# Kernel tuning notes

Measured on AMD Instinct MI355X. Metric: run time of the kernel, lower is better.

## Reference

```python
import jax, jax.numpy as jnp
import numpy as np

N_NODES = 100000
N_EDGES = 1600000
IN_F = 128
OUT_F = 128
HID = 2 * OUT_F  # 256


def setup_inputs() -> dict:
    key = jax.random.key(0)
    k1, k2, k3, k4, k5 = jax.random.split(key, 5)
    x = jax.random.normal(k1, (N_NODES, IN_F), dtype=jnp.float32)
    src = jax.random.randint(k2, (N_EDGES,), 0, N_NODES, dtype=jnp.int64)
    dst = jax.random.randint(k3, (N_EDGES,), 0, N_NODES, dtype=jnp.int64)
    # GraphConv params: glorot-style init, zero bias (as in dgl defaults)
    W1 = jax.random.normal(k4, (IN_F, HID), dtype=jnp.float32) / np.sqrt(IN_F)
    b1 = jnp.zeros((HID,), dtype=jnp.float32)
    W2 = jax.random.normal(k5, (HID, OUT_F), dtype=jnp.float32) / np.sqrt(HID)
    b2 = jnp.zeros((OUT_F,), dtype=jnp.float32)
    return {"x": x, "W1": W1, "b1": b1, "W2": W2, "b2": b2, "src": src, "dst": dst}


def _degree_norms(src, dst):
    ones = jnp.ones(src.shape[0], dtype=jnp.float32)
    out_deg = jax.ops.segment_sum(ones, src, num_segments=N_NODES)
    in_deg = jax.ops.segment_sum(ones, dst, num_segments=N_NODES)
    # dgl norm='both': deg^{-1/2}, with 0-degree clamped to 1
    out_norm = jnp.where(out_deg > 0, out_deg, 1.0) ** -0.5
    in_norm = jnp.where(in_deg > 0, in_deg, 1.0) ** -0.5
    return out_norm, in_norm


def _graph_conv(x, W, b, src, dst, out_norm, in_norm):
    # dgl GraphConv, norm='both': apply weight first if in_feats > out_feats
    h = x * out_norm[:, None]
    if W.shape[0] > W.shape[1]:
        h = h @ W                       # [N, out] -- shrink before aggregation
        agg = jax.ops.segment_sum(h[src], dst, num_segments=N_NODES)
        return agg * in_norm[:, None] + b
    else:
        agg = jax.ops.segment_sum(h[src], dst, num_segments=N_NODES)
        return (agg * in_norm[:, None]) @ W + b


def reference(x, W1, b1, W2, b2, src, dst):
    out_norm, in_norm = _degree_norms(src, dst)
    h = jax.nn.relu(_graph_conv(x, W1, b1, src, dst, out_norm, in_norm))
    h = jax.nn.relu(_graph_conv(h, W2, b2, src, dst, out_norm, in_norm))
    return h
```

## Files before the change

### kernel.cpp

```cpp
#include <hip/hip_runtime.h>
#include <stdint.h>

#define NNODES 100000
#define NEDGES 1600000
#define NBIN 391
#define EPB 4096
#define NB 391

typedef unsigned short bf16_t;
typedef __attribute__((ext_vector_type(8))) short bf16x8;
typedef __attribute__((ext_vector_type(8))) unsigned short u16x8;
typedef __attribute__((ext_vector_type(4))) float f32x4;

__device__ __forceinline__ float bf2f(unsigned short u) {
  return __uint_as_float(((unsigned)u) << 16);
}
__device__ __forceinline__ unsigned short f2bf(float f) {
  unsigned u = __float_as_uint(f);
  return (unsigned short)((u + 0x7FFFu + ((u >> 16) & 1u)) >> 16);
}
__device__ __forceinline__ void gload_lds16(const void* g, void* lds) {
  __builtin_amdgcn_global_load_lds(
      (const __attribute__((address_space(1))) unsigned int*)g,
      (__attribute__((address_space(3))) unsigned int*)lds, 16, 0, 0);
}

__global__ __launch_bounds__(256) void hist2_kernel(
    const int* __restrict__ src, const int* __restrict__ dst,
    int* __restrict__ cntD, int* __restrict__ cntS) {
  __shared__ int hD[NBIN], hS[NBIN];
  int blk = blockIdx.x, t = threadIdx.x;
  for (int i = t; i < NBIN; i += 256) { hD[i] = 0; hS[i] = 0; }
  __syncthreads();
  int e0 = blk * EPB + t * 16;
  if (e0 + 15 < NEDGES) {
#pragma unroll
    for (int q = 0; q < 4; q++) {
      int4 s4 = *reinterpret_cast<const int4*>(src + e0 + q * 4);
      int4 d4 = *reinterpret_cast<const int4*>(dst + e0 + q * 4);
      atomicAdd(&hD[d4.x >> 8], 1); atomicAdd(&hS[s4.x >> 8], 1);
      atomicAdd(&hD[d4.y >> 8], 1); atomicAdd(&hS[s4.y >> 8], 1);
      atomicAdd(&hD[d4.z >> 8], 1); atomicAdd(&hS[s4.z >> 8], 1);
      atomicAdd(&hD[d4.w >> 8], 1); atomicAdd(&hS[s4.w >> 8], 1);
    }
  } else {
    for (int e = e0; e < NEDGES && e < e0 + 16; e++) {
      atomicAdd(&hD[dst[e] >> 8], 1);
      atomicAdd(&hS[src[e] >> 8], 1);
    }
  }
  __syncthreads();
  for (int i = t; i < NBIN; i += 256) {
    cntD[(size_t)blk * NBIN + i] = hD[i];
    cntS[(size_t)blk * NBIN + i] = hS[i];
  }
}

__global__ __launch_bounds__(512) void scan_bin_kernel(
    int* __restrict__ cntD, int* __restrict__ cntS, int* __restrict__ binTot) {
  __shared__ int lds[512];
  int g = blockIdx.x, t = threadIdx.x;
  int* cnt = (g < NBIN) ? cntD : cntS;
  int gg = (g < NBIN) ? g : g - NBIN;
  int v = (t < NB) ? cnt[(size_t)t * NBIN + gg] : 0;
  lds[t] = v;
  __syncthreads();
  for (int off = 1; off < 512; off <<= 1) {
    int a = (t >= off) ? lds[t - off] : 0;
    __syncthreads();
    lds[t] += a;
    __syncthreads();
  }
  if (t < NB) cnt[(size_t)t * NBIN + gg] = lds[t] - v;
  if (t == 0) binTot[g] = lds[511];
}

__global__ __launch_bounds__(512) void base_wcast_kernel(
    const int* __restrict__ binTot, int* __restrict__ binbaseD,
    int* __restrict__ binbaseS, int* __restrict__ row_ptr,
    const float* __restrict__ W1, const float* __restrict__ W2,
    bf16_t* __restrict__ W1t, bf16_t* __restrict__ W2t) {
  if (blockIdx.x == 0) {
    __shared__ int lds[512];
    int t = threadIdx.x;
    int v = (t < NBIN) ? binTot[t] : 0;
    lds[t] = v;
    __syncthreads();
    for (int off = 1; off < 512; off <<= 1) {
      int a = (t >= off) ? lds[t - off] : 0;
      __syncthreads();
      lds[t] += a;
      __syncthreads();
    }
    if (t < NBIN) binbaseD[t] = lds[t] - v;
    if (t == NBIN - 1) { binbaseD[NBIN] = lds[t]; row_ptr[NNODES] = lds[t]; }
    __syncthreads();
    int v2 = (t < NBIN) ? binTot[NBIN + t] : 0;
    lds[t] = v2;
    __syncthreads();
    for (int off = 1; off < 512; off <<= 1) {
      int a = (t >= off) ? lds[t - off] : 0;
      __syncthreads();
      lds[t] += a;
      __syncthreads();
    }
    if (t < NBIN) binbaseS[t] = lds[t] - v2;
    if (t == NBIN - 1) binbaseS[NBIN] = lds[t];
  } else {
    int i = (blockIdx.x - 1) * 512 + threadIdx.x;
    if (i < 32768) {
      int n = i / 128, k = i % 128;
      W1t[i] = f2bf(W1[(size_t)k * 256 + n]);
    } else if (i < 65536) {
      int j = i - 32768;
      int n = j / 256, k = j % 256;
      W2t[j] = f2bf(W2[(size_t)k * 128 + n]);
    }
  }
}

__global__ __launch_bounds__(256) void scatter_recs_kernel(
    const int* __restrict__ src, const int* __restrict__ dst,
    const int* __restrict__ cntD, const int* __restrict__ cntS,
    const int* __restrict__ binbaseD, const int* __restrict__ binbaseS,
    unsigned int* __restrict__ recD, unsigned char* __restrict__ recS) {
  __shared__ int cD[NBIN], cS[NBIN];
  int blk = blockIdx.x, t = threadIdx.x;
  for (int i = t; i < NBIN; i += 256) {
    cD[i] = binbaseD[i] + cntD[(size_t)blk * NBIN + i];
    cS[i] = binbaseS[i] + cntS[(size_t)blk * NBIN + i];
  }
  __syncthreads();
  int e0 = blk * EPB + t * 16;
  if (e0 + 15 < NEDGES) {
#pragma unroll
    for (int q = 0; q < 4; q++) {
      int4 s4 = *reinterpret_cast<const int4*>(src + e0 + q * 4);
      int4 d4 = *reinterpret_cast<const int4*>(dst + e0 + q * 4);
      int ss[4] = {s4.x, s4.y, s4.z, s4.w};
      int dd[4] = {d4.x, d4.y, d4.z, d4.w};
#pragma unroll
      for (int i = 0; i < 4; i++) {
        int s = ss[i], d = dd[i];
        int pos = atomicAdd(&cD[d >> 8], 1);
        recD[pos] = ((unsigned)s << 8) | (unsigned)(d & 255);
        int ps = atomicAdd(&cS[s >> 8], 1);
        recS[ps] = (unsigned char)(s & 255);
      }
    }
  } else {
    for (int e = e0; e < NEDGES && e < e0 + 16; e++) {
      int s = src[e], d = dst[e];
      int pos = atomicAdd(&cD[d >> 8], 1);
      recD[pos] = ((unsigned)s << 8) | (unsigned)(d & 255);
      int ps = atomicAdd(&cS[s >> 8], 1);
      recS[ps] = (unsigned char)(s & 255);
    }
  }
}

__global__ __launch_bounds__(512) void finish2_kernel(
    const unsigned int* __restrict__ recD, const int* __restrict__ binbaseD,
    const unsigned char* __restrict__ recS, const int* __restrict__ binbaseS,
    int* __restrict__ row_ptr, float* __restrict__ in_norm, int* __restrict__ csr,
    float* __restrict__ out_norm, const float* __restrict__ x, bf16_t* __restrict__ xb) {
  __shared__ int hist[4096];
  __shared__ int cur[4096];
  __shared__ int sc[512];
  __shared__ float onv[256];
  int t = threadIdx.x;
  if (blockIdx.x < NBIN) {
    int b = blockIdx.x;
    int base = binbaseD[b];
    int cnt = binbaseD[b + 1] - base;
    for (int i = t; i < 4096; i += 512) hist[i] = 0;
    __syncthreads();
    const unsigned int* rec = recD + base;
    for (int i = t; i < cnt; i += 512) {
      unsigned int r = rec[i];
      atomicAdd(&hist[((r & 255u) << 4) | (r >> 21)], 1);
    }
    __syncthreads();
    int loc[8];
    int lsum = 0;
#pragma unroll
    for (int i = 0; i < 8; i++) { loc[i] = lsum; lsum += hist[t * 8 + i]; }
    sc[t] = lsum;
    __syncthreads();
    for (int off = 1; off < 512; off <<= 1) {
      int a = (t >= off) ? sc[t - off] : 0;
      __syncthreads();
      sc[t] += a;
      __syncthreads();
    }
    int toff = sc[t] - lsum;
#pragma unroll
    for (int i = 0; i < 8; i++) cur[t * 8 + i] = base + toff + loc[i];
    __syncthreads();
    if (t < 256) {
      int n = (b << 8) + t;
      if (n < NNODES) {
        row_ptr[n] = cur[t * 16];
        int v = 0;
#pragma unroll
        for (int p = 0; p < 16; p++) v += hist[t * 16 + p];
        in_norm[n] = rsqrtf((float)(v > 0 ? v : 1));
      }
    }
    __syncthreads();
    for (int i = t; i < cnt; i += 512) {
      unsigned int r = rec[i];
      int key = ((r & 255u) << 4) | (r >> 21);
      int slot = atomicAdd(&cur[key], 1);
      csr[slot] = (int)(r >> 8);
    }
  } else {
    int b = blockIdx.x - NBIN;
    int base = binbaseS[b];
    int cnt = binbaseS[b + 1] - base;
    if (t < 256) hist[t] = 0;
    __syncthreads();
    const unsigned char* rec = recS + base;
    for (int i = t; i < cnt; i += 512) atomicAdd(&hist[rec[i]], 1);
    __syncthreads();
    int n0 = b << 8;
    if (t < 256) {
      int v = hist[t];
      float on = rsqrtf((float)(v > 0 ? v : 1));
      onv[t] = on;
      int n = n0 + t;
      if (n < NNODES) out_norm[n] = on;
    }
    __syncthreads();
    for (int idx = t; idx < 256 * 16; idx += 512) {
      int r16 = idx >> 4, chunk = idx & 15;
      int n = n0 + r16;
      if (n >= NNODES) break;
      float s = onv[r16];
      const float4* xp = reinterpret_cast<const float4*>(x + (size_t)n * 128 + chunk * 8);
      float4 v0 = xp[0], v1 = xp[1];
      u16x8 u;
      u[0] = f2bf(v0.x * s); u[1] = f2bf(v0.y * s); u[2] = f2bf(v0.z * s); u[3] = f2bf(v0.w * s);
      u[4] = f2bf(v1.x * s); u[5] = f2bf(v1.y * s); u[6] = f2bf(v1.z * s); u[7] = f2bf(v1.w * s);
      *reinterpret_cast<u16x8*>(xb + (size_t)n * 128 + chunk * 8) = u;
    }
  }
}

template <int FIN>
__global__ __launch_bounds__(256) void gather_kernel(
    const bf16_t* __restrict__ feat, const int* __restrict__ row_ptr,
    const int* __restrict__ csr, const float* __restrict__ rs,
    const float* __restrict__ bias, void* __restrict__ outp) {
  int nbk = gridDim.x;
  int q = nbk >> 3, r = nbk & 7;
  int x = blockIdx.x & 7, o = blockIdx.x >> 3;
  int vb = (x < r ? x * (q + 1) : r * (q + 1) + (x - r) * q) + o;
  int node = vb * 16 + (threadIdx.x >> 4);
  int lane = threadIdx.x & 15;
  int start = row_ptr[node];
  int end = row_ptr[node + 1];
  float a[8];
#pragma unroll
  for (int t = 0; t < 8; t++) a[t] = 0.f;
  int j = start;
  for (; j + 7 < end; j += 8) {
    int4 sa = *reinterpret_cast<const int4*>(csr + j);
    int4 sb = *reinterpret_cast<const int4*>(csr + j + 4);
    u16x8 u0 = *reinterpret_cast<const u16x8*>(feat + (size_t)sa.x * 128 + lane * 8);
    u16x8 u1 = *reinterpret_cast<const u16x8*>(feat + (size_t)sa.y * 128 + lane * 8);
    u16x8 u2 = *reinterpret_cast<const u16x8*>(feat + (size_t)sa.z * 128 + lane * 8);
    u16x8 u3 = *reinterpret_cast<const u16x8*>(feat + (size_t)sa.w * 128 + lane * 8);
    u16x8 u4 = *reinterpret_cast<const u16x8*>(feat + (size_t)sb.x * 128 + lane * 8);
    u16x8 u5 = *reinterpret_cast<const u16x8*>(feat + (size_t)sb.y * 128 + lane * 8);
    u16x8 u6 = *reinterpret_cast<const u16x8*>(feat + (size_t)sb.z * 128 + lane * 8);
    u16x8 u7 = *reinterpret_cast<const u16x8*>(feat + (size_t)sb.w * 128 + lane * 8);
#pragma unroll
    for (int t = 0; t < 8; t++)
      a[t] += ((bf2f((unsigned short)u0[t]) + bf2f((unsigned short)u1[t])) +
               (bf2f((unsigned short)u2[t]) + bf2f((unsigned short)u3[t]))) +
              ((bf2f((unsigned short)u4[t]) + bf2f((unsigned short)u5[t])) +
               (bf2f((unsigned short)u6[t]) + bf2f((unsigned short)u7[t])));
  }
  if (j + 3 < end) {
    int4 sa = *reinterpret_cast<const int4*>(csr + j);
    u16x8 u0 = *reinterpret_cast<const u16x8*>(feat + (size_t)sa.x * 128 + lane * 8);
    u16x8 u1 = *reinterpret_cast<const u16x8*>(feat + (size_t)sa.y * 128 + lane * 8);
    u16x8 u2 = *reinterpret_cast<const u16x8*>(feat + (size_t)sa.z * 128 + lane * 8);
    u16x8 u3 = *reinterpret_cast<const u16x8*>(feat + (size_t)sa.w * 128 + lane * 8);
#pragma unroll
    for (int t = 0; t < 8; t++)
      a[t] += (bf2f((unsigned short)u0[t]) + bf2f((unsigned short)u1[t])) +
              (bf2f((unsigned short)u2[t]) + bf2f((unsigned short)u3[t]));
    j += 4;
  }
  for (; j < end; j++) {
    int s0 = csr[j];
    u16x8 u0 = *reinterpret_cast<const u16x8*>(feat + (size_t)s0 * 128 + lane * 8);
#pragma unroll
    for (int t = 0; t < 8; t++) a[t] += bf2f((unsigned short)u0[t]);
  }
  if (FIN == 0) {
    u16x8 o8;
#pragma unroll
    for (int t = 0; t < 8; t++) o8[t] = f2bf(a[t]);
    *reinterpret_cast<u16x8*>((bf16_t*)outp + (size_t)node * 128 + lane * 8) = o8;
  } else {
    float s = rs[node];
    const float* bp = bias + lane * 8;
    float4 o0, o1;
    o0.x = fmaxf(fmaf(a[0], s, bp[0]), 0.f);
    o0.y = fmaxf(fmaf(a[1], s, bp[1]), 0.f);
    o0.z = fmaxf(fmaf(a[2], s, bp[2]), 0.f);
    o0.w = fmaxf(fmaf(a[3], s, bp[3]), 0.f);
    o1.x = fmaxf(fmaf(a[4], s, bp[4]), 0.f);
    o1.y = fmaxf(fmaf(a[5], s, bp[5]), 0.f);
    o1.z = fmaxf(fmaf(a[6], s, bp[6]), 0.f);
    o1.w = fmaxf(fmaf(a[7], s, bp[7]), 0.f);
    float* op = (float*)outp + (size_t)node * 128 + lane * 8;
    *reinterpret_cast<float4*>(op) = o0;
    *reinterpret_cast<float4*>(op + 4) = o1;
  }
}

__global__ __launch_bounds__(256) void gemm12_kernel(
    const bf16_t* __restrict__ A,
    const bf16_t* __restrict__ W1t,
    const bf16_t* __restrict__ W2t,
    const float* __restrict__ b1,
    const float* __restrict__ in_norm,
    const float* __restrict__ out_norm,
    bf16_t* __restrict__ s2b) {
  __shared__ __align__(16) bf16_t As[64 * 128];
  __shared__ __align__(16) bf16_t Wb[128 * 128];
  __shared__ __align__(16) bf16_t H[64 * 256];

  const int tid = threadIdx.x;
  const int lane = tid & 63;
  const int w = tid >> 6;
  const int m0 = blockIdx.x * 64;
  const int l15 = lane & 15;
  const int S = lane >> 4;
  const int r = w * 16 + l15;
  const int lr0 = w * 16 + S * 4;

#pragma unroll
  for (int p = 0; p < 4; p++) {
    int pos = p * 256 + tid;
    int rr = pos >> 4, slot = pos & 15;
    int row = m0 + rr; if (row > NNODES - 1) row = NNODES - 1;
    int ko = (slot ^ (rr & 7)) << 3;
    gload_lds16(A + (size_t)row * 128 + ko, &As[(p * 256 + w * 64) * 8]);
  }
#pragma unroll
  for (int p = 0; p < 8; p++) {
    int pos = p * 256 + tid;
    int n = pos >> 4, slot = pos & 15;
    int ko = (slot ^ (n & 7)) << 3;
    gload_lds16(W1t + (size_t)n * 128 + ko, &Wb[(p * 256 + w * 64) * 8]);
  }
  __syncthreads();

  float inn[4];
#pragma unroll
  for (int reg = 0; reg < 4; reg++) {
    int grow = m0 + lr0 + reg;
    inn[reg] = (grow < NNODES) ? in_norm[grow] : 1.0f;
  }

#pragma unroll
  for (int h = 0; h < 2; h++) {
    if (h == 1) {
      __syncthreads();
#pragma unroll
      for (int p = 0; p < 8; p++) {
        int pos = p * 256 + tid;
        int n = pos >> 4, slot = pos & 15;
        int ko = (slot ^ (n & 7)) << 3;
        gload_lds16(W1t + (size_t)(128 + n) * 128 + ko, &Wb[(p * 256 + w * 64) * 8]);
      }
      __syncthreads();
    }
    f32x4 acc1[8];
#pragma unroll
    for (int fn = 0; fn < 8; fn++) acc1[fn] = (f32x4){0.f, 0.f, 0.f, 0.f};
#pragma unroll
    for (int kk8 = 0; kk8 < 16; kk8 += 4) {
      bf16x8 af = *reinterpret_cast<const bf16x8*>(&As[r * 128 + (((kk8 + S) ^ (r & 7)) << 3)]);
#pragma unroll
      for (int fn = 0; fn < 8; fn++) {
        int n = fn * 16 + l15;
        bf16x8 bf = *reinterpret_cast<const bf16x8*>(&Wb[n * 128 + (((kk8 + S) ^ (n & 7)) << 3)]);
        acc1[fn] = __builtin_amdgcn_mfma_f32_16x16x32_bf16(af, bf, acc1[fn], 0, 0, 0);
      }
    }
#pragma unroll
    for (int fn = 0; fn < 8; fn++) {
      int col = h * 128 + fn * 16 + l15;
      float bb = b1[col];
#pragma unroll
      for (int reg = 0; reg < 4; reg++) {
        int lr = lr0 + reg;
        float v = fmaxf(fmaf(acc1[fn][reg], inn[reg], bb), 0.f);
        int slot = (col >> 3) ^ (lr & 7);
        H[lr * 256 + slot * 8 + (col & 7)] = f2bf(v);
      }
    }
  }
  __syncthreads();

  f32x4 acc2[8];
#pragma unroll
  for (int fn = 0; fn < 8; fn++) acc2[fn] = (f32x4){0.f, 0.f, 0.f, 0.f};
#pragma unroll
  for (int kh = 0; kh < 2; kh++) {
#pragma unroll
    for (int p = 0; p < 8; p++) {
      int pos = p * 256 + tid;
      int n = pos >> 4, slot = pos & 15;
      int ko = kh * 128 + ((slot ^ (n & 7)) << 3);
      gload_lds16(W2t + (size_t)n * 256 + ko, &Wb[(p * 256 + w * 64) * 8]);
    }
    __syncthreads();
#pragma unroll
    for (int kk8 = 0; kk8 < 16; kk8 += 4) {
      int oct = kh * 16 + kk8 + S;
      bf16x8 af = *reinterpret_cast<const bf16x8*>(&H[r * 256 + ((oct ^ (r & 7)) << 3)]);
#pragma unroll
      for (int fn = 0; fn < 8; fn++) {
        int n = fn * 16 + l15;
        bf16x8 bf = *reinterpret_cast<const bf16x8*>(&Wb[n * 128 + (((kk8 + S) ^ (n & 7)) << 3)]);
        acc2[fn] = __builtin_amdgcn_mfma_f32_16x16x32_bf16(af, bf, acc2[fn], 0, 0, 0);
      }
    }
    __syncthreads();
  }

  float onr[4];
#pragma unroll
  for (int reg = 0; reg < 4; reg++) {
    int grow = m0 + lr0 + reg;
    onr[reg] = (grow < NNODES) ? out_norm[grow] : 0.0f;
  }
#pragma unroll
  for (int fn = 0; fn < 8; fn++) {
    int col = fn * 16 + l15;
#pragma unroll
    for (int reg = 0; reg < 4; reg++) {
      int lr = lr0 + reg;
      As[lr * 128 + col] = f2bf(acc2[fn][reg] * onr[reg]);
    }
  }
  __syncthreads();
#pragma unroll
  for (int p = 0; p < 4; p++) {
    int pos = p * 256 + tid;
    int rr = pos >> 4;
    int cc = (pos & 15) * 8;
    int grow = m0 + rr;
    if (grow < NNODES)
      *reinterpret_cast<u16x8*>(s2b + (size_t)grow * 128 + cc) =
          *reinterpret_cast<const u16x8*>(&As[rr * 128 + cc]);
  }
}

extern "C" void kernel_launch(void* const* d_in, const int* in_sizes, int n_in,
                              void* d_out, int out_size, void* d_ws, size_t ws_size,
                              hipStream_t stream) {
  const float* x  = (const float*)d_in[0];
  const float* W1 = (const float*)d_in[1];
  const float* b1 = (const float*)d_in[2];
  const float* W2 = (const float*)d_in[3];
  const float* b2 = (const float*)d_in[4];
  const int* src  = (const int*)d_in[5];
  const int* dst  = (const int*)d_in[6];
  float* out = (float*)d_out;

  char* ws = (char*)d_ws;
  int*           cntD     = (int*)          (ws + 0);
  int*           cntS     = (int*)          (ws + 700000);
  int*           binTot   = (int*)          (ws + 1400000);
  int*           binbaseD = (int*)          (ws + 1404000);
  int*           binbaseS = (int*)          (ws + 1406000);
  int*           row_ptr  = (int*)          (ws + 1408000);
  float*         out_norm = (float*)        (ws + 1810000);
  float*         in_norm  = (float*)        (ws + 2210000);
  bf16_t*        W1t      = (bf16_t*)       (ws + 2610000);
  bf16_t*        W2t      = (bf16_t*)       (ws + 2675536);
  unsigned int*  recD     = (unsigned int*) (ws + 2741072);
  unsigned char* recS     = (unsigned char*)(ws + 9141072);
  int*           csr      = (int*)          (ws + 10741072);
  bf16_t*        xb       = (bf16_t*)       (ws + 17141072);
  bf16_t*        agg1     = (bf16_t*)       (ws + 42741072);
  bf16_t*        s2b      = xb;

  hist2_kernel<<<NB, 256, 0, stream>>>(src, dst, cntD, cntS);
  scan_bin_kernel<<<2 * NBIN, 512, 0, stream>>>(cntD, cntS, binTot);
  base_wcast_kernel<<<129, 512, 0, stream>>>(binTot, binbaseD, binbaseS, row_ptr, W1, W2, W1t, W2t);
  scatter_recs_kernel<<<NB, 256, 0, stream>>>(src, dst, cntD, cntS, binbaseD, binbaseS, recD, recS);
  finish2_kernel<<<2 * NBIN, 512, 0, stream>>>(recD, binbaseD, recS, binbaseS,
                                               row_ptr, in_norm, csr, out_norm, x, xb);

  gather_kernel<0><<<NNODES / 16, 256, 0, stream>>>(xb, row_ptr, csr, nullptr, nullptr, agg1);

  gemm12_kernel<<<(NNODES + 63) / 64, 256, 0, stream>>>(agg1, W1t, W2t, b1, in_norm, out_norm, s2b);

  gather_kernel<1><<<NNODES / 16, 256, 0, stream>>>(s2b, row_ptr, csr, in_norm, b2, out);
}
```

Measured before the change: 255.2 us.

## Fuse first-layer gather with both dense GEMMs into one kernel

The first aggregation is merged with the two MFMA matmuls in one kernel. Each 16-node block keeps its aggregated row tile in LDS and multiplies it by W1 and then W2, reading the weights directly from global memory instead of staging them in LDS. This removes the bf16 agg1 round-trip to HBM and one kernel launch. In exchange, every block re-reads W1t and W2t (relying on L2 hits), runs only 16-row MFMA tiles, and the extra LDS may lower occupancy of the latency-bound gather.

```diff
diff --git a/kernel.cpp b/kernel.cpp
--- a/kernel.cpp
+++ b/kernel.cpp
@@ -247,17 +247,27 @@
   }
 }
 
-template <int FIN>
-__global__ __launch_bounds__(256) void gather_kernel(
-    const bf16_t* __restrict__ feat, const int* __restrict__ row_ptr,
-    const int* __restrict__ csr, const float* __restrict__ rs,
-    const float* __restrict__ bias, void* __restrict__ outp) {
+__global__ __launch_bounds__(256) void gather_gemm_kernel(
+    const bf16_t* __restrict__ feat,
+    const int* __restrict__ row_ptr, const int* __restrict__ csr,
+    const bf16_t* __restrict__ W1t,
+    const bf16_t* __restrict__ W2t,
+    const float* __restrict__ b1,
+    const float* __restrict__ in_norm,
+    const float* __restrict__ out_norm,
+    bf16_t* __restrict__ s2b) {
+  __shared__ __align__(16) bf16_t T[16 * 128];
+  __shared__ __align__(16) bf16_t H[16 * 256];
+
   int nbk = gridDim.x;
-  int q = nbk >> 3, r = nbk & 7;
-  int x = blockIdx.x & 7, o = blockIdx.x >> 3;
-  int vb = (x < r ? x * (q + 1) : r * (q + 1) + (x - r) * q) + o;
-  int node = vb * 16 + (threadIdx.x >> 4);
+  int q = nbk >> 3, r8 = nbk & 7;
+  int xc = blockIdx.x & 7, ob = blockIdx.x >> 3;
+  int vb = (xc < r8 ? xc * (q + 1) : r8 * (q + 1) + (xc - r8) * q) + ob;
+  int node0 = vb * 16;
+  int g = threadIdx.x >> 4;
   int lane = threadIdx.x & 15;
+  int node = node0 + g;
+
   int start = row_ptr[node];
   int end = row_ptr[node + 1];
   float a[8];
@@ -300,168 +310,154 @@
 #pragma unroll
     for (int t = 0; t < 8; t++) a[t] += bf2f((unsigned short)u0[t]);
   }
-  if (FIN == 0) {
+  {
     u16x8 o8;
 #pragma unroll
     for (int t = 0; t < 8; t++) o8[t] = f2bf(a[t]);
-    *reinterpret_cast<u16x8*>((bf16_t*)outp + (size_t)node * 128 + lane * 8) = o8;
-  } else {
-    float s = rs[node];
-    const float* bp = bias + lane * 8;
-    float4 o0, o1;
-    o0.x = fmaxf(fmaf(a[0], s, bp[0]), 0.f);
-    o0.y = fmaxf(fmaf(a[1], s, bp[1]), 0.f);
-    o0.z = fmaxf(fmaf(a[2], s, bp[2]), 0.f);
-    o0.w = fmaxf(fmaf(a[3], s, bp[3]), 0.f);
-    o1.x = fmaxf(fmaf(a[4], s, bp[4]), 0.f);
-    o1.y = fmaxf(fmaf(a[5], s, bp[5]), 0.f);
-    o1.z = fmaxf(fmaf(a[6], s, bp[6]), 0.f);
-    o1.w = fmaxf(fmaf(a[7], s, bp[7]), 0.f);
-    float* op = (float*)outp + (size_t)node * 128 + lane * 8;
-    *reinterpret_cast<float4*>(op) = o0;
-    *reinterpret_cast<float4*>(op + 4) = o1;
-  }
-}
-
-__global__ __launch_bounds__(256) void gemm12_kernel(
-    const bf16_t* __restrict__ A,
-    const bf16_t* __restrict__ W1t,
-    const bf16_t* __restrict__ W2t,
-    const float* __restrict__ b1,
-    const float* __restrict__ in_norm,
-    const float* __restrict__ out_norm,
-    bf16_t* __restrict__ s2b) {
-  __shared__ __align__(16) bf16_t As[64 * 128];
-  __shared__ __align__(16) bf16_t Wb[128 * 128];
-  __shared__ __align__(16) bf16_t H[64 * 256];
+    *reinterpret_cast<u16x8*>(&T[g * 128 + ((lane ^ (g & 7)) << 3)]) = o8;
+  }
+  __syncthreads();
 
   const int tid = threadIdx.x;
-  const int lane = tid & 63;
-  const int w = tid >> 6;
-  const int m0 = blockIdx.x * 64;
-  const int l15 = lane & 15;
-  const int S = lane >> 4;
-  const int r = w * 16 + l15;
-  const int lr0 = w * 16 + S * 4;
-
-#pragma unroll
-  for (int p = 0; p < 4; p++) {
-    int pos = p * 256 + tid;
-    int rr = pos >> 4, slot = pos & 15;
-    int row = m0 + rr; if (row > NNODES - 1) row = NNODES - 1;
-    int ko = (slot ^ (rr & 7)) << 3;
-    gload_lds16(A + (size_t)row * 128 + ko, &As[(p * 256 + w * 64) * 8]);
-  }
-#pragma unroll
-  for (int p = 0; p < 8; p++) {
-    int pos = p * 256 + tid;
-    int n = pos >> 4, slot = pos & 15;
-    int ko = (slot ^ (n & 7)) << 3;
-    gload_lds16(W1t + (size_t)n * 128 + ko, &Wb[(p * 256 + w * 64) * 8]);
-  }
-  __syncthreads();
-
-  float inn[4];
+  const int wv = tid >> 6;
+  const int l63 = tid & 63;
+  const int l15 = l63 & 15;
+  const int S = l63 >> 4;
+  const int row0 = S * 4;
+
+  float inn[4], onr[4];
 #pragma unroll
   for (int reg = 0; reg < 4; reg++) {
-    int grow = m0 + lr0 + reg;
-    inn[reg] = (grow < NNODES) ? in_norm[grow] : 1.0f;
-  }
-
-#pragma unroll
-  for (int h = 0; h < 2; h++) {
-    if (h == 1) {
-      __syncthreads();
-#pragma unroll
-      for (int p = 0; p < 8; p++) {
-        int pos = p * 256 + tid;
-        int n = pos >> 4, slot = pos & 15;
-        int ko = (slot ^ (n & 7)) << 3;
-        gload_lds16(W1t + (size_t)(128 + n) * 128 + ko, &Wb[(p * 256 + w * 64) * 8]);
-      }
-      __syncthreads();
-    }
-    f32x4 acc1[8];
-#pragma unroll
-    for (int fn = 0; fn < 8; fn++) acc1[fn] = (f32x4){0.f, 0.f, 0.f, 0.f};
-#pragma unroll
-    for (int kk8 = 0; kk8 < 16; kk8 += 4) {
-      bf16x8 af = *reinterpret_cast<const bf16x8*>(&As[r * 128 + (((kk8 + S) ^ (r & 7)) << 3)]);
-#pragma unroll
-      for (int fn = 0; fn < 8; fn++) {
-        int n = fn * 16 + l15;
-        bf16x8 bf = *reinterpret_cast<const bf16x8*>(&Wb[n * 128 + (((kk8 + S) ^ (n & 7)) << 3)]);
-        acc1[fn] = __builtin_amdgcn_mfma_f32_16x16x32_bf16(af, bf, acc1[fn], 0, 0, 0);
-      }
-    }
-#pragma unroll
-    for (int fn = 0; fn < 8; fn++) {
-      int col = h * 128 + fn * 16 + l15;
-      float bb = b1[col];
-#pragma unroll
-      for (int reg = 0; reg < 4; reg++) {
-        int lr = lr0 + reg;
-        float v = fmaxf(fmaf(acc1[fn][reg], inn[reg], bb), 0.f);
-        int slot = (col >> 3) ^ (lr & 7);
-        H[lr * 256 + slot * 8 + (col & 7)] = f2bf(v);
-      }
-    }
-  }
-  __syncthreads();
-
-  f32x4 acc2[8];
-#pragma unroll
-  for (int fn = 0; fn < 8; fn++) acc2[fn] = (f32x4){0.f, 0.f, 0.f, 0.f};
-#pragma unroll
-  for (int kh = 0; kh < 2; kh++) {
-#pragma unroll
-    for (int p = 0; p < 8; p++) {
-      int pos = p * 256 + tid;
-      int n = pos >> 4, slot = pos & 15;
-      int ko = kh * 128 + ((slot ^ (n & 7)) << 3);
-      gload_lds16(W2t + (size_t)n * 256 + ko, &Wb[(p * 256 + w * 64) * 8]);
-    }
-    __syncthreads();
-#pragma unroll
-    for (int kk8 = 0; kk8 < 16; kk8 += 4) {
-      int oct = kh * 16 + kk8 + S;
-      bf16x8 af = *reinterpret_cast<const bf16x8*>(&H[r * 256 + ((oct ^ (r & 7)) << 3)]);
-#pragma unroll
-      for (int fn = 0; fn < 8; fn++) {
-        int n = fn * 16 + l15;
-        bf16x8 bf = *reinterpret_cast<const bf16x8*>(&Wb[n * 128 + (((kk8 + S) ^ (n & 7)) << 3)]);
-        acc2[fn] = __builtin_amdgcn_mfma_f32_16x16x32_bf16(af, bf, acc2[fn], 0, 0, 0);
-      }
-    }
-    __syncthreads();
-  }
-
-  float onr[4];
-#pragma unroll
-  for (int reg = 0; reg < 4; reg++) {
-    int grow = m0 + lr0 + reg;
-    onr[reg] = (grow < NNODES) ? out_norm[grow] : 0.0f;
-  }
-#pragma unroll
-  for (int fn = 0; fn < 8; fn++) {
-    int col = fn * 16 + l15;
+    inn[reg] = in_norm[node0 + row0 + reg];
+    onr[reg] = out_norm[node0 + row0 + reg];
+  }
+
+  f32x4 acc1[4];
+#pragma unroll
+  for (int fn = 0; fn < 4; fn++) acc1[fn] = (f32x4){0.f, 0.f, 0.f, 0.f};
+#pragma unroll
+  for (int ks = 0; ks < 4; ks++) {
+    int oct = ks * 4 + S;
+    bf16x8 af = *reinterpret_cast<const bf16x8*>(&T[l15 * 128 + ((oct ^ (l15 & 7)) << 3)]);
+#pragma unroll
+    for (int fn = 0; fn < 4; fn++) {
+      int n = wv * 64 + fn * 16 + l15;
+      bf16x8 bf = *reinterpret_cast<const bf16x8*>(W1t + (size_t)n * 128 + oct * 8);
+      acc1[fn] = __builtin_amdgcn_mfma_f32_16x16x32_bf16(af, bf, acc1[fn], 0, 0, 0);
+    }
+  }
+#pragma unroll
+  for (int fn = 0; fn < 4; fn++) {
+    int col = wv * 64 + fn * 16 + l15;
+    float bb = b1[col];
 #pragma unroll
     for (int reg = 0; reg < 4; reg++) {
-      int lr = lr0 + reg;
-      As[lr * 128 + col] = f2bf(acc2[fn][reg] * onr[reg]);
-    }
-  }
-  __syncthreads();
-#pragma unroll
-  for (int p = 0; p < 4; p++) {
-    int pos = p * 256 + tid;
-    int rr = pos >> 4;
-    int cc = (pos & 15) * 8;
-    int grow = m0 + rr;
-    if (grow < NNODES)
-      *reinterpret_cast<u16x8*>(s2b + (size_t)grow * 128 + cc) =
-          *reinterpret_cast<const u16x8*>(&As[rr * 128 + cc]);
-  }
+      int lr = row0 + reg;
+      float v = fmaxf(fmaf(acc1[fn][reg], inn[reg], bb), 0.f);
+      int slot = (col >> 3) ^ (lr & 7);
+      H[lr * 256 + slot * 8 + (col & 7)] = f2bf(v);
+    }
+  }
+  __syncthreads();
+
+  f32x4 acc2[2];
+#pragma unroll
+  for (int fn = 0; fn < 2; fn++) acc2[fn] = (f32x4){0.f, 0.f, 0.f, 0.f};
+#pragma unroll
+  for (int ks = 0; ks < 8; ks++) {
+    int oct = ks * 4 + S;
+    bf16x8 af = *reinterpret_cast<const bf16x8*>(&H[l15 * 256 + ((oct ^ (l15 & 7)) << 3)]);
+#pragma unroll
+    for (int fn = 0; fn < 2; fn++) {
+      int n = wv * 32 + fn * 16 + l15;
+      bf16x8 bf = *reinterpret_cast<const bf16x8*>(W2t + (size_t)n * 256 + oct * 8);
+      acc2[fn] = __builtin_amdgcn_mfma_f32_16x16x32_bf16(af, bf, acc2[fn], 0, 0, 0);
+    }
+  }
+  __syncthreads();
+#pragma unroll
+  for (int fn = 0; fn < 2; fn++) {
+    int col = wv * 32 + fn * 16 + l15;
+#pragma unroll
+    for (int reg = 0; reg < 4; reg++) {
+      int lr = row0 + reg;
+      T[lr * 128 + col] = f2bf(acc2[fn][reg] * onr[reg]);
+    }
+  }
+  __syncthreads();
+  {
+    int rr = tid >> 4, cc = (tid & 15) * 8;
+    *reinterpret_cast<u16x8*>(s2b + (size_t)(node0 + rr) * 128 + cc) =
+        *reinterpret_cast<const u16x8*>(&T[rr * 128 + cc]);
+  }
+}
+
+__global__ __launch_bounds__(256) void gather_kernel(
+    const bf16_t* __restrict__ feat, const int* __restrict__ row_ptr,
+    const int* __restrict__ csr, const float* __restrict__ rs,
+    const float* __restrict__ bias, float* __restrict__ outp) {
+  int nbk = gridDim.x;
+  int q = nbk >> 3, r = nbk & 7;
+  int x = blockIdx.x & 7, o = blockIdx.x >> 3;
+  int vb = (x < r ? x * (q + 1) : r * (q + 1) + (x - r) * q) + o;
+  int node = vb * 16 + (threadIdx.x >> 4);
+  int lane = threadIdx.x & 15;
+  int start = row_ptr[node];
+  int end = row_ptr[node + 1];
+  float a[8];
+#pragma unroll
+  for (int t = 0; t < 8; t++) a[t] = 0.f;
+  int j = start;
+  for (; j + 7 < end; j += 8) {
+    int4 sa = *reinterpret_cast<const int4*>(csr + j);
+    int4 sb = *reinterpret_cast<const int4*>(csr + j + 4);
+    u16x8 u0 = *reinterpret_cast<const u16x8*>(feat + (size_t)sa.x * 128 + lane * 8);
+    u16x8 u1 = *reinterpret_cast<const u16x8*>(feat + (size_t)sa.y * 128 + lane * 8);
+    u16x8 u2 = *reinterpret_cast<const u16x8*>(feat + (size_t)sa.z * 128 + lane * 8);
+    u16x8 u3 = *reinterpret_cast<const u16x8*>(feat + (size_t)sa.w * 128 + lane * 8);
+    u16x8 u4 = *reinterpret_cast<const u16x8*>(feat + (size_t)sb.x * 128 + lane * 8);
+    u16x8 u5 = *reinterpret_cast<const u16x8*>(feat + (size_t)sb.y * 128 + lane * 8);
+    u16x8 u6 = *reinterpret_cast<const u16x8*>(feat + (size_t)sb.z * 128 + lane * 8);
+    u16x8 u7 = *reinterpret_cast<const u16x8*>(feat + (size_t)sb.w * 128 + lane * 8);
+#pragma unroll
+    for (int t = 0; t < 8; t++)
+      a[t] += ((bf2f((unsigned short)u0[t]) + bf2f((unsigned short)u1[t])) +
+               (bf2f((unsigned short)u2[t]) + bf2f((unsigned short)u3[t]))) +
+              ((bf2f((unsigned short)u4[t]) + bf2f((unsigned short)u5[t])) +
+               (bf2f((unsigned short)u6[t]) + bf2f((unsigned short)u7[t])));
+  }
+  if (j + 3 < end) {
+    int4 sa = *reinterpret_cast<const int4*>(csr + j);
+    u16x8 u0 = *reinterpret_cast<const u16x8*>(feat + (size_t)sa.x * 128 + lane * 8);
+    u16x8 u1 = *reinterpret_cast<const u16x8*>(feat + (size_t)sa.y * 128 + lane * 8);
+    u16x8 u2 = *reinterpret_cast<const u16x8*>(feat + (size_t)sa.z * 128 + lane * 8);
+    u16x8 u3 = *reinterpret_cast<const u16x8*>(feat + (size_t)sa.w * 128 + lane * 8);
+#pragma unroll
+    for (int t = 0; t < 8; t++)
+      a[t] += (bf2f((unsigned short)u0[t]) + bf2f((unsigned short)u1[t])) +
+              (bf2f((unsigned short)u2[t]) + bf2f((unsigned short)u3[t]));
+    j += 4;
+  }
+  for (; j < end; j++) {
+    int s0 = csr[j];
+    u16x8 u0 = *reinterpret_cast<const u16x8*>(feat + (size_t)s0 * 128 + lane * 8);
+#pragma unroll
+    for (int t = 0; t < 8; t++) a[t] += bf2f((unsigned short)u0[t]);
+  }
+  float s = rs[node];
+  const float* bp = bias + lane * 8;
+  float4 o0, o1;
+  o0.x = fmaxf(fmaf(a[0], s, bp[0]), 0.f);
+  o0.y = fmaxf(fmaf(a[1], s, bp[1]), 0.f);
+  o0.z = fmaxf(fmaf(a[2], s, bp[2]), 0.f);
+  o0.w = fmaxf(fmaf(a[3], s, bp[3]), 0.f);
+  o1.x = fmaxf(fmaf(a[4], s, bp[4]), 0.f);
+  o1.y = fmaxf(fmaf(a[5], s, bp[5]), 0.f);
+  o1.z = fmaxf(fmaf(a[6], s, bp[6]), 0.f);
+  o1.w = fmaxf(fmaf(a[7], s, bp[7]), 0.f);
+  float* op = outp + (size_t)node * 128 + lane * 8;
+  *reinterpret_cast<float4*>(op) = o0;
+  *reinterpret_cast<float4*>(op + 4) = o1;
 }
 
 extern "C" void kernel_launch(void* const* d_in, const int* in_sizes, int n_in,
@@ -491,8 +487,7 @@
   unsigned char* recS     = (unsigned char*)(ws + 9141072);
   int*           csr      = (int*)          (ws + 10741072);
   bf16_t*        xb       = (bf16_t*)       (ws + 17141072);
-  bf16_t*        agg1     = (bf16_t*)       (ws + 42741072);
-  bf16_t*        s2b      = xb;
+  bf16_t*        s2b      = (bf16_t*)       (ws + 42741072);
 
   hist2_kernel<<<NB, 256, 0, stream>>>(src, dst, cntD, cntS);
   scan_bin_kernel<<<2 * NBIN, 512, 0, stream>>>(cntD, cntS, binTot);
@@ -501,9 +496,8 @@
   finish2_kernel<<<2 * NBIN, 512, 0, stream>>>(recD, binbaseD, recS, binbaseS,
                                                row_ptr, in_norm, csr, out_norm, x, xb);
 
-  gather_kernel<0><<<NNODES / 16, 256, 0, stream>>>(xb, row_ptr, csr, nullptr, nullptr, agg1);
-
-  gemm12_kernel<<<(NNODES + 63) / 64, 256, 0, stream>>>(agg1, W1t, W2t, b1, in_norm, out_norm, s2b);
-
-  gather_kernel<1><<<NNODES / 16, 256, 0, stream>>>(s2b, row_ptr, csr, in_norm, b2, out);
-}
+  gather_gemm_kernel<<<NNODES / 16, 256, 0, stream>>>(xb, row_ptr, csr, W1t, W2t,
+                                                      b1, in_norm, out_norm, s2b);
+
+  gather_kernel<<<NNODES / 16, 256, 0, stream>>>(s2b, row_ptr, csr, in_norm, b2, out);
+}
```

New measurement: 286.2 us. 12.2% more time.

## Replace per-block bin counts and scan with global atomic bin totals and cursors

Applied to the files above, without the earlier changes.

The histogram kernel now adds per-block bin counts straight into global bin totals with atomics, which removes the per-block count arrays and the separate column-scan kernel. The scatter kernel recomputes its local histogram and reserves each block's offsets by atomically bumping global per-bin cursors, so edge order within a bin is no longer deterministic. The gather kernel also switches its CSR index loads and output stores to nontemporal accesses. The aim is to cut one launch and the intermediate count traffic, at the cost of redoing the histogram pass and adding global atomic contention.

```diff
diff --git a/kernel.cpp b/kernel.cpp
--- a/kernel.cpp
+++ b/kernel.cpp
@@ -11,6 +11,7 @@
 typedef __attribute__((ext_vector_type(8))) short bf16x8;
 typedef __attribute__((ext_vector_type(8))) unsigned short u16x8;
 typedef __attribute__((ext_vector_type(4))) float f32x4;
+typedef __attribute__((ext_vector_type(4))) int i32x4;
 
 __device__ __forceinline__ float bf2f(unsigned short u) {
   return __uint_as_float(((unsigned)u) << 16);
@@ -25,9 +26,9 @@
       (__attribute__((address_space(3))) unsigned int*)lds, 16, 0, 0);
 }
 
-__global__ __launch_bounds__(256) void hist2_kernel(
+__global__ __launch_bounds__(256) void histg_kernel(
     const int* __restrict__ src, const int* __restrict__ dst,
-    int* __restrict__ cntD, int* __restrict__ cntS) {
+    int* __restrict__ binTot) {
   __shared__ int hD[NBIN], hS[NBIN];
   int blk = blockIdx.x, t = threadIdx.x;
   for (int i = t; i < NBIN; i += 256) { hD[i] = 0; hS[i] = 0; }
@@ -51,33 +52,15 @@
   }
   __syncthreads();
   for (int i = t; i < NBIN; i += 256) {
-    cntD[(size_t)blk * NBIN + i] = hD[i];
-    cntS[(size_t)blk * NBIN + i] = hS[i];
-  }
-}
-
-__global__ __launch_bounds__(512) void scan_bin_kernel(
-    int* __restrict__ cntD, int* __restrict__ cntS, int* __restrict__ binTot) {
-  __shared__ int lds[512];
-  int g = blockIdx.x, t = threadIdx.x;
-  int* cnt = (g < NBIN) ? cntD : cntS;
-  int gg = (g < NBIN) ? g : g - NBIN;
-  int v = (t < NB) ? cnt[(size_t)t * NBIN + gg] : 0;
-  lds[t] = v;
-  __syncthreads();
-  for (int off = 1; off < 512; off <<= 1) {
-    int a = (t >= off) ? lds[t - off] : 0;
-    __syncthreads();
-    lds[t] += a;
-    __syncthreads();
-  }
-  if (t < NB) cnt[(size_t)t * NBIN + gg] = lds[t] - v;
-  if (t == 0) binTot[g] = lds[511];
+    if (hD[i]) atomicAdd(&binTot[i], hD[i]);
+    if (hS[i]) atomicAdd(&binTot[NBIN + i], hS[i]);
+  }
 }
 
 __global__ __launch_bounds__(512) void base_wcast_kernel(
     const int* __restrict__ binTot, int* __restrict__ binbaseD,
-    int* __restrict__ binbaseS, int* __restrict__ row_ptr,
+    int* __restrict__ binbaseS, int* __restrict__ cursD, int* __restrict__ cursS,
+    int* __restrict__ row_ptr,
     const float* __restrict__ W1, const float* __restrict__ W2,
     bf16_t* __restrict__ W1t, bf16_t* __restrict__ W2t) {
   if (blockIdx.x == 0) {
@@ -92,7 +75,7 @@
       lds[t] += a;
       __syncthreads();
     }
-    if (t < NBIN) binbaseD[t] = lds[t] - v;
+    if (t < NBIN) { int b = lds[t] - v; binbaseD[t] = b; cursD[t] = b; }
     if (t == NBIN - 1) { binbaseD[NBIN] = lds[t]; row_ptr[NNODES] = lds[t]; }
     __syncthreads();
     int v2 = (t < NBIN) ? binTot[NBIN + t] : 0;
@@ -104,7 +87,7 @@
       lds[t] += a;
       __syncthreads();
     }
-    if (t < NBIN) binbaseS[t] = lds[t] - v2;
+    if (t < NBIN) { int b = lds[t] - v2; binbaseS[t] = b; cursS[t] = b; }
     if (t == NBIN - 1) binbaseS[NBIN] = lds[t];
   } else {
     int i = (blockIdx.x - 1) * 512 + threadIdx.x;
@@ -119,19 +102,39 @@
   }
 }
 
-__global__ __launch_bounds__(256) void scatter_recs_kernel(
+__global__ __launch_bounds__(256) void scatter2_kernel(
     const int* __restrict__ src, const int* __restrict__ dst,
-    const int* __restrict__ cntD, const int* __restrict__ cntS,
-    const int* __restrict__ binbaseD, const int* __restrict__ binbaseS,
+    int* __restrict__ cursD, int* __restrict__ cursS,
     unsigned int* __restrict__ recD, unsigned char* __restrict__ recS) {
-  __shared__ int cD[NBIN], cS[NBIN];
+  __shared__ int hD[NBIN], hS[NBIN];
   int blk = blockIdx.x, t = threadIdx.x;
+  for (int i = t; i < NBIN; i += 256) { hD[i] = 0; hS[i] = 0; }
+  __syncthreads();
+  int e0 = blk * EPB + t * 16;
+  if (e0 + 15 < NEDGES) {
+#pragma unroll
+    for (int q = 0; q < 4; q++) {
+      int4 s4 = *reinterpret_cast<const int4*>(src + e0 + q * 4);
+      int4 d4 = *reinterpret_cast<const int4*>(dst + e0 + q * 4);
+      atomicAdd(&hD[d4.x >> 8], 1); atomicAdd(&hS[s4.x >> 8], 1);
+      atomicAdd(&hD[d4.y >> 8], 1); atomicAdd(&hS[s4.y >> 8], 1);
+      atomicAdd(&hD[d4.z >> 8], 1); atomicAdd(&hS[s4.z >> 8], 1);
+      atomicAdd(&hD[d4.w >> 8], 1); atomicAdd(&hS[s4.w >> 8], 1);
+    }
+  } else {
+    for (int e = e0; e < NEDGES && e < e0 + 16; e++) {
+      atomicAdd(&hD[dst[e] >> 8], 1);
+      atomicAdd(&hS[src[e] >> 8], 1);
+    }
+  }
+  __syncthreads();
   for (int i = t; i < NBIN; i += 256) {
-    cD[i] = binbaseD[i] + cntD[(size_t)blk * NBIN + i];
-    cS[i] = binbaseS[i] + cntS[(size_t)blk * NBIN + i];
-  }
-  __syncthreads();
-  int e0 = blk * EPB + t * 16;
+    int c = hD[i];
+    hD[i] = c ? atomicAdd(&cursD[i], c) : 0;
+    int c2 = hS[i];
+    hS[i] = c2 ? atomicAdd(&cursS[i], c2) : 0;
+  }
+  __syncthreads();
   if (e0 + 15 < NEDGES) {
 #pragma unroll
     for (int q = 0; q < 4; q++) {
@@ -142,18 +145,18 @@
 #pragma unroll
       for (int i = 0; i < 4; i++) {
         int s = ss[i], d = dd[i];
-        int pos = atomicAdd(&cD[d >> 8], 1);
+        int pos = atomicAdd(&hD[d >> 8], 1);
         recD[pos] = ((unsigned)s << 8) | (unsigned)(d & 255);
-        int ps = atomicAdd(&cS[s >> 8], 1);
+        int ps = atomicAdd(&hS[s >> 8], 1);
         recS[ps] = (unsigned char)(s & 255);
       }
     }
   } else {
     for (int e = e0; e < NEDGES && e < e0 + 16; e++) {
       int s = src[e], d = dst[e];
-      int pos = atomicAdd(&cD[d >> 8], 1);
+      int pos = atomicAdd(&hD[d >> 8], 1);
       recD[pos] = ((unsigned)s << 8) | (unsigned)(d & 255);
-      int ps = atomicAdd(&cS[s >> 8], 1);
+      int ps = atomicAdd(&hS[s >> 8], 1);
       recS[ps] = (unsigned char)(s & 255);
     }
   }
@@ -265,16 +268,16 @@
   for (int t = 0; t < 8; t++) a[t] = 0.f;
   int j = start;
   for (; j + 7 < end; j += 8) {
-    int4 sa = *reinterpret_cast<const int4*>(csr + j);
-    int4 sb = *reinterpret_cast<const int4*>(csr + j + 4);
-    u16x8 u0 = *reinterpret_cast<const u16x8*>(feat + (size_t)sa.x * 128 + lane * 8);
-    u16x8 u1 = *reinterpret_cast<const u16x8*>(feat + (size_t)sa.y * 128 + lane * 8);
-    u16x8 u2 = *reinterpret_cast<const u16x8*>(feat + (size_t)sa.z * 128 + lane * 8);
-    u16x8 u3 = *reinterpret_cast<const u16x8*>(feat + (size_t)sa.w * 128 + lane * 8);
-    u16x8 u4 = *reinterpret_cast<const u16x8*>(feat + (size_t)sb.x * 128 + lane * 8);
-    u16x8 u5 = *reinterpret_cast<const u16x8*>(feat + (size_t)sb.y * 128 + lane * 8);
-    u16x8 u6 = *reinterpret_cast<const u16x8*>(feat + (size_t)sb.z * 128 + lane * 8);
-    u16x8 u7 = *reinterpret_cast<const u16x8*>(feat + (size_t)sb.w * 128 + lane * 8);
+    i32x4 sa = __builtin_nontemporal_load(reinterpret_cast<const i32x4*>(csr + j));
+    i32x4 sb = __builtin_nontemporal_load(reinterpret_cast<const i32x4*>(csr + j + 4));
+    u16x8 u0 = *reinterpret_cast<const u16x8*>(feat + (size_t)sa[0] * 128 + lane * 8);
+    u16x8 u1 = *reinterpret_cast<const u16x8*>(feat + (size_t)sa[1] * 128 + lane * 8);
+    u16x8 u2 = *reinterpret_cast<const u16x8*>(feat + (size_t)sa[2] * 128 + lane * 8);
+    u16x8 u3 = *reinterpret_cast<const u16x8*>(feat + (size_t)sa[3] * 128 + lane * 8);
+    u16x8 u4 = *reinterpret_cast<const u16x8*>(feat + (size_t)sb[0] * 128 + lane * 8);
+    u16x8 u5 = *reinterpret_cast<const u16x8*>(feat + (size_t)sb[1] * 128 + lane * 8);
+    u16x8 u6 = *reinterpret_cast<const u16x8*>(feat + (size_t)sb[2] * 128 + lane * 8);
+    u16x8 u7 = *reinterpret_cast<const u16x8*>(feat + (size_t)sb[3] * 128 + lane * 8);
 #pragma unroll
     for (int t = 0; t < 8; t++)
       a[t] += ((bf2f((unsigned short)u0[t]) + bf2f((unsigned short)u1[t])) +
@@ -283,11 +286,11 @@
                (bf2f((unsigned short)u6[t]) + bf2f((unsigned short)u7[t])));
   }
   if (j + 3 < end) {
-    int4 sa = *reinterpret_cast<const int4*>(csr + j);
-    u16x8 u0 = *reinterpret_cast<const u16x8*>(feat + (size_t)sa.x * 128 + lane * 8);
-    u16x8 u1 = *reinterpret_cast<const u16x8*>(feat + (size_t)sa.y * 128 + lane * 8);
-    u16x8 u2 = *reinterpret_cast<const u16x8*>(feat + (size_t)sa.z * 128 + lane * 8);
-    u16x8 u3 = *reinterpret_cast<const u16x8*>(feat + (size_t)sa.w * 128 + lane * 8);
+    i32x4 sa = __builtin_nontemporal_load(reinterpret_cast<const i32x4*>(csr + j));
+    u16x8 u0 = *reinterpret_cast<const u16x8*>(feat + (size_t)sa[0] * 128 + lane * 8);
+    u16x8 u1 = *reinterpret_cast<const u16x8*>(feat + (size_t)sa[1] * 128 + lane * 8);
+    u16x8 u2 = *reinterpret_cast<const u16x8*>(feat + (size_t)sa[2] * 128 + lane * 8);
+    u16x8 u3 = *reinterpret_cast<const u16x8*>(feat + (size_t)sa[3] * 128 + lane * 8);
 #pragma unroll
     for (int t = 0; t < 8; t++)
       a[t] += (bf2f((unsigned short)u0[t]) + bf2f((unsigned short)u1[t])) +
@@ -304,22 +307,23 @@
     u16x8 o8;
 #pragma unroll
     for (int t = 0; t < 8; t++) o8[t] = f2bf(a[t]);
-    *reinterpret_cast<u16x8*>((bf16_t*)outp + (size_t)node * 128 + lane * 8) = o8;
+    __builtin_nontemporal_store(
+        o8, reinterpret_cast<u16x8*>((bf16_t*)outp + (size_t)node * 128 + lane * 8));
   } else {
     float s = rs[node];
     const float* bp = bias + lane * 8;
-    float4 o0, o1;
-    o0.x = fmaxf(fmaf(a[0], s, bp[0]), 0.f);
-    o0.y = fmaxf(fmaf(a[1], s, bp[1]), 0.f);
-    o0.z = fmaxf(fmaf(a[2], s, bp[2]), 0.f);
-    o0.w = fmaxf(fmaf(a[3], s, bp[3]), 0.f);
-    o1.x = fmaxf(fmaf(a[4], s, bp[4]), 0.f);
-    o1.y = fmaxf(fmaf(a[5], s, bp[5]), 0.f);
-    o1.z = fmaxf(fmaf(a[6], s, bp[6]), 0.f);
-    o1.w = fmaxf(fmaf(a[7], s, bp[7]), 0.f);
+    f32x4 o0, o1;
+    o0[0] = fmaxf(fmaf(a[0], s, bp[0]), 0.f);
+    o0[1] = fmaxf(fmaf(a[1], s, bp[1]), 0.f);
+    o0[2] = fmaxf(fmaf(a[2], s, bp[2]), 0.f);
+    o0[3] = fmaxf(fmaf(a[3], s, bp[3]), 0.f);
+    o1[0] = fmaxf(fmaf(a[4], s, bp[4]), 0.f);
+    o1[1] = fmaxf(fmaf(a[5], s, bp[5]), 0.f);
+    o1[2] = fmaxf(fmaf(a[6], s, bp[6]), 0.f);
+    o1[3] = fmaxf(fmaf(a[7], s, bp[7]), 0.f);
     float* op = (float*)outp + (size_t)node * 128 + lane * 8;
-    *reinterpret_cast<float4*>(op) = o0;
-    *reinterpret_cast<float4*>(op + 4) = o1;
+    __builtin_nontemporal_store(o0, reinterpret_cast<f32x4*>(op));
+    __builtin_nontemporal_store(o1, reinterpret_cast<f32x4*>(op + 4));
   }
 }
 
@@ -477,27 +481,29 @@
   float* out = (float*)d_out;
 
   char* ws = (char*)d_ws;
-  int*           cntD     = (int*)          (ws + 0);
-  int*           cntS     = (int*)          (ws + 700000);
-  int*           binTot   = (int*)          (ws + 1400000);
-  int*           binbaseD = (int*)          (ws + 1404000);
-  int*           binbaseS = (int*)          (ws + 1406000);
-  int*           row_ptr  = (int*)          (ws + 1408000);
-  float*         out_norm = (float*)        (ws + 1810000);
-  float*         in_norm  = (float*)        (ws + 2210000);
-  bf16_t*        W1t      = (bf16_t*)       (ws + 2610000);
-  bf16_t*        W2t      = (bf16_t*)       (ws + 2675536);
-  unsigned int*  recD     = (unsigned int*) (ws + 2741072);
-  unsigned char* recS     = (unsigned char*)(ws + 9141072);
-  int*           csr      = (int*)          (ws + 10741072);
-  bf16_t*        xb       = (bf16_t*)       (ws + 17141072);
-  bf16_t*        agg1     = (bf16_t*)       (ws + 42741072);
+  int*           binTot   = (int*)          (ws + 0);
+  int*           binbaseD = (int*)          (ws + 4000);
+  int*           binbaseS = (int*)          (ws + 6000);
+  int*           cursD    = (int*)          (ws + 8000);
+  int*           cursS    = (int*)          (ws + 10000);
+  int*           row_ptr  = (int*)          (ws + 12000);
+  float*         out_norm = (float*)        (ws + 420000);
+  float*         in_norm  = (float*)        (ws + 830000);
+  bf16_t*        W1t      = (bf16_t*)       (ws + 1240000);
+  bf16_t*        W2t      = (bf16_t*)       (ws + 1305536);
+  unsigned int*  recD     = (unsigned int*) (ws + 1371072);
+  unsigned char* recS     = (unsigned char*)(ws + 7771072);
+  int*           csr      = (int*)          (ws + 9371072);
+  bf16_t*        xb       = (bf16_t*)       (ws + 15771072);
+  bf16_t*        agg1     = (bf16_t*)       (ws + 41371072);
   bf16_t*        s2b      = xb;
 
-  hist2_kernel<<<NB, 256, 0, stream>>>(src, dst, cntD, cntS);
-  scan_bin_kernel<<<2 * NBIN, 512, 0, stream>>>(cntD, cntS, binTot);
-  base_wcast_kernel<<<129, 512, 0, stream>>>(binTot, binbaseD, binbaseS, row_ptr, W1, W2, W1t, W2t);
-  scatter_recs_kernel<<<NB, 256, 0, stream>>>(src, dst, cntD, cntS, binbaseD, binbaseS, recD, recS);
+  hipMemsetAsync(binTot, 0, 2 * NBIN * sizeof(int), stream);
+
+  histg_kernel<<<NB, 256, 0, stream>>>(src, dst, binTot);
+  base_wcast_kernel<<<129, 512, 0, stream>>>(binTot, binbaseD, binbaseS, cursD, cursS,
+                                             row_ptr, W1, W2, W1t, W2t);
+  scatter2_kernel<<<NB, 256, 0, stream>>>(src, dst, cursD, cursS, recD, recS);
   finish2_kernel<<<2 * NBIN, 512, 0, stream>>>(recD, binbaseD, recS, binbaseS,
                                                row_ptr, in_norm, csr, out_norm, x, xb);
 
```

After: 281.2 us. 10.2% more time.
